# Kernel optimization log

Measured on AMD Instinct MI355X. Metric: run time of the kernel, lower is better.

Reference implementation:

```python
import jax, jax.numpy as jnp
import numpy as np
import math

B, S, H, D = 8, 4096, 768, 64  # batch, seq_len, hidden_dim, head_size


def setup_inputs() -> dict:
    key = jax.random.key(0)
    kx, kk, kq, kv, kbk, kbq, kbv = jax.random.split(key, 7)
    s = 1.0 / math.sqrt(H)
    return {
        "x": jax.random.normal(kx, (B, S, H), dtype=jnp.float32),
        "Wk": jax.random.normal(kk, (H, D), dtype=jnp.float32) * s,
        "bk": jax.random.normal(kbk, (D,), dtype=jnp.float32) * s,
        "Wq": jax.random.normal(kq, (H, D), dtype=jnp.float32) * s,
        "bq": jax.random.normal(kbq, (D,), dtype=jnp.float32) * s,
        "Wv": jax.random.normal(kv, (H, D), dtype=jnp.float32) * s,
        "bv": jax.random.normal(kbv, (D,), dtype=jnp.float32) * s,
    }


def reference(x, Wk, bk, Wq, bq, Wv, bv):
    # projections: [B, S, D]
    k = x @ Wk + bk
    q = x @ Wq + bq
    v = x @ Wv + bv
    # full O(S^2) attention scores, as in the original module
    weight = jnp.einsum("bqd,bkd->bqk", q, k)  # [B, S, S]
    causal = jnp.tril(jnp.ones((S, S), dtype=bool))
    # original masks first, then divides by sqrt(head_size); -inf/sqrt = -inf
    weight = jnp.where(causal, weight, -jnp.inf) / math.sqrt(D)
    weight = jax.nn.softmax(weight, axis=-1)
    # dropout p=0.0 (eval-mode reference): identity
    out = jnp.einsum("bqk,bkd->bqd", weight, v)  # [B, S, D]
    return out
```

## Files before the change

### kernel.cpp

```cpp
#include <hip/hip_runtime.h>
#include <hip/hip_bf16.h>
#include <math.h>

#define B_ 8
#define S_ 4096
#define H_ 768
#define D_ 64

typedef __bf16 bf16;
typedef bf16 bf16x8 __attribute__((ext_vector_type(8)));
typedef bf16 bf16x4 __attribute__((ext_vector_type(4)));
typedef float floatx4 __attribute__((ext_vector_type(4)));

__device__ __forceinline__ int sw_off(int r, int chunk) {
    return r * 128 + ((chunk ^ (r & 7)) << 4);
}
__device__ __forceinline__ int sw_elem(int r, int e) {
    return r * 64 + (((e >> 3) ^ (r & 7)) << 3) + (e & 7);
}

__device__ __forceinline__ void dma16(const bf16* gsrc, bf16* ldst) {
    __builtin_amdgcn_global_load_lds(
        (const __attribute__((address_space(1))) unsigned int*)(const void*)gsrc,
        (__attribute__((address_space(3))) unsigned int*)(void*)ldst,
        16, 0, 0);
}

__global__ __launch_bounds__(256) void wtrans_kernel(
    const float* __restrict__ Wq, const float* __restrict__ Wk,
    const float* __restrict__ Wv, bf16* __restrict__ wt)
{
    __shared__ bf16 t_lds[64][72];
    const float* W = (blockIdx.y == 0) ? Wq : (blockIdx.y == 1) ? Wk : Wv;
    bf16* o = wt + ((size_t)blockIdx.y * 12 + blockIdx.x) * 4096;
    const int k0 = blockIdx.x * 64;
    const int tid = threadIdx.x;
    #pragma unroll
    for (int rep = 0; rep < 16; ++rep) {
        int idx = rep * 256 + tid;
        int r = idx >> 6, n = idx & 63;
        t_lds[n][r] = (bf16)W[(size_t)(k0 + r) * D_ + n];
    }
    __syncthreads();
    #pragma unroll
    for (int rep = 0; rep < 16; ++rep) {
        int idx = rep * 256 + tid;
        int n = idx >> 6, kk = idx & 63;
        o[sw_elem(n, kk)] = t_lds[n][kk];
    }
}

__global__ __launch_bounds__(256, 2) void proj_kernel(
    const float* __restrict__ x, const bf16* __restrict__ wt,
    const float* __restrict__ bq, const float* __restrict__ bk,
    const float* __restrict__ bv,
    bf16* __restrict__ qout, bf16* __restrict__ kout, bf16* __restrict__ vtt)
{
    __shared__ bf16 wlds[2][3][4096];

    const int m0   = blockIdx.x * 64;
    const int tid  = threadIdx.x;
    const int lane = tid & 63;
    const int wave = tid >> 6;
    const int quad = lane >> 4;
    const int c    = lane & 15;
    const int mrow = m0 + wave * 16 + c;

    floatx4 acc[3][4] = {};
    const float* xrow = &x[(size_t)mrow * H_ + quad * 8];

    auto loadA = [&](int k0, bf16x8* dst) {
        #pragma unroll
        for (int s = 0; s < 2; ++s) {
            const float* xp = xrow + k0 + s * 32;
            float4 f0 = *(const float4*)xp;
            float4 f1 = *(const float4*)(xp + 4);
            bf16x8 a;
            a[0] = (bf16)f0.x; a[1] = (bf16)f0.y; a[2] = (bf16)f0.z; a[3] = (bf16)f0.w;
            a[4] = (bf16)f1.x; a[5] = (bf16)f1.y; a[6] = (bf16)f1.z; a[7] = (bf16)f1.w;
            dst[s] = a;
        }
    };
    auto stageW = [&](int kt, int buf) {
        #pragma unroll
        for (int w = 0; w < 3; ++w) {
            const bf16* src = wt + (size_t)(w * 12 + kt) * 4096 + wave * 1024 + lane * 8;
            bf16* dst = &wlds[buf][w][wave * 1024];
            dma16(src, dst);
            dma16(src + 512, dst + 512);
        }
    };

    bf16x8 afn[2]; loadA(0, afn);
    stageW(0, 0);

    for (int kt = 0; kt < 12; ++kt) {
        __syncthreads();
        const int cur = kt & 1;
        if (kt < 11) stageW(kt + 1, 1 - cur);
        bf16x8 af[2] = { afn[0], afn[1] };
        if (kt < 11) loadA((kt + 1) * 64, afn);
        #pragma unroll
        for (int s = 0; s < 2; ++s)
            #pragma unroll
            for (int w = 0; w < 3; ++w)
                #pragma unroll
                for (int tn = 0; tn < 4; ++tn) {
                    bf16x8 bfrag = *(const bf16x8*)
                        ((const char*)&wlds[cur][w][0] + sw_off(tn * 16 + c, s * 4 + quad));
                    acc[w][tn] = __builtin_amdgcn_mfma_f32_16x16x32_bf16(
                        af[s], bfrag, acc[w][tn], 0, 0, 0);
                }
    }

    const int rbase = m0 + wave * 16 + quad * 4;
    const int bb = m0 >> 12;
    const int jt = (m0 & 4095) >> 6;
    const size_t tbase = ((size_t)bb * 64 + jt) * 4096;
    #pragma unroll
    for (int tn = 0; tn < 4; ++tn) {
        const int n = tn * 16 + c;
        float bqv = bq[n];
        #pragma unroll
        for (int r = 0; r < 4; ++r)
            qout[(size_t)(rbase + r) * 128 + n] = (bf16)(acc[0][tn][r] + bqv);
        float bkv = bk[n];
        #pragma unroll
        for (int r = 0; r < 4; ++r) {
            const int sl = (rbase & 63) + r;
            kout[tbase + sw_elem(sl, n)] = (bf16)(acc[1][tn][r] + bkv);
        }
        float bvv = bv[n];
        bf16x4 pk;
        #pragma unroll
        for (int r = 0; r < 4; ++r) pk[r] = (bf16)(acc[2][tn][r] + bvv);
        const int sl0 = (rbase & 63);
        *(bf16x4*)&vtt[tbase + sw_elem(n, sl0)] = pk;
    }
}

__global__ __launch_bounds__(128, 2) void attn_kernel(
    const bf16* __restrict__ q, const bf16* __restrict__ k,
    const bf16* __restrict__ vt, float* __restrict__ out)
{
    __shared__ bf16 klds[2][4096];
    __shared__ bf16 vlds[2][4096];
    __shared__ bf16 plds[2][1024];

    const int tid  = threadIdx.x;
    const int lane = tid & 63;
    const int wave = tid >> 6;
    const int quad = lane >> 4;
    const int c    = lane & 15;
    const int i    = blockIdx.x;
    const int slot = i >> 8;
    const int cc   = i & 255;
    const int b    = cc & 7;
    const int x    = cc >> 3;
    const int qt   = (slot == 0) ? (127 - x) : (slot == 1) ? x
                   : (slot == 2) ? (95 - x)  : (32 + x);
    const int jmax = qt >> 1;
    const int qrow = qt * 32 + wave * 16;
    const float cl = 0.18033688011112042f;
    const float M2 = 16.0f;

    const bf16* ktile0 = k  + (size_t)b * 64 * 4096;
    const bf16* vtile0 = vt + (size_t)b * 64 * 4096;
    bf16* pl = &plds[wave][0];

    auto stage = [&](const bf16* gsrc, bf16* ldst) {
        const bf16* s = gsrc + wave * 2048 + lane * 8;
        bf16* d = ldst + wave * 2048;
        #pragma unroll
        for (int n = 0; n < 4; ++n) dma16(s + n * 512, d + n * 512);
    };

    bf16x8 qf[2];
    #pragma unroll
    for (int s = 0; s < 2; ++s)
        qf[s] = *(const bf16x8*)
            &q[(size_t)(b * S_ + qrow + c) * 128 + s * 32 + quad * 8];

    floatx4 acc_o[4] = {};
    float lpart[4] = {0.f, 0.f, 0.f, 0.f};

    stage(ktile0, klds[0]);
    stage(vtile0, vlds[0]);

    #pragma unroll 1
    for (int j = 0; j <= jmax; ++j) {
        __syncthreads();
        const int cur = j & 1;
        if (j < jmax) {
            stage(ktile0 + (size_t)(j + 1) * 4096, klds[1 - cur]);
            stage(vtile0 + (size_t)(j + 1) * 4096, vlds[1 - cur]);
        }

        floatx4 sa[4] = {};
        #pragma unroll
        for (int s = 0; s < 2; ++s)
            #pragma unroll
            for (int tn = 0; tn < 4; ++tn) {
                bf16x8 kf = *(const bf16x8*)
                    ((const char*)&klds[cur][0] + sw_off(tn * 16 + c, s * 4 + quad));
                sa[tn] = __builtin_amdgcn_mfma_f32_16x16x32_bf16(qf[s], kf, sa[tn], 0, 0, 0);
            }

        if (j == jmax) {
            #pragma unroll
            for (int tn = 0; tn < 4; ++tn) {
                const int col = j * 64 + tn * 16 + c;
                #pragma unroll
                for (int r = 0; r < 4; ++r)
                    if (col > qrow + quad * 4 + r) sa[tn][r] = -INFINITY;
            }
        }

        #pragma unroll
        for (int tn = 0; tn < 4; ++tn)
            #pragma unroll
            for (int r = 0; r < 4; ++r) {
                float p = __builtin_amdgcn_exp2f(fmaf(sa[tn][r], cl, -M2));
                sa[tn][r] = p;
                lpart[r] += p;
            }

        bf16x8 vf[2][4];
        #pragma unroll
        for (int s = 0; s < 2; ++s)
            #pragma unroll
            for (int tn = 0; tn < 4; ++tn)
                vf[s][tn] = *(const bf16x8*)
                    ((const char*)&vlds[cur][0] + sw_off(tn * 16 + c, s * 4 + quad));

        #pragma unroll
        for (int tn = 0; tn < 4; ++tn)
            #pragma unroll
            for (int r = 0; r < 4; ++r)
                pl[sw_elem(quad * 4 + r, tn * 16 + c)] = (bf16)sa[tn][r];

        bf16x8 pf[2];
        #pragma unroll
        for (int s = 0; s < 2; ++s)
            pf[s] = *(const bf16x8*)((const char*)pl + sw_off(c, s * 4 + quad));

        #pragma unroll
        for (int s = 0; s < 2; ++s)
            #pragma unroll
            for (int tn = 0; tn < 4; ++tn)
                acc_o[tn] = __builtin_amdgcn_mfma_f32_16x16x32_bf16(pf[s], vf[s][tn], acc_o[tn], 0, 0, 0);
    }

    #pragma unroll
    for (int r = 0; r < 4; ++r) {
        lpart[r] += __shfl_xor(lpart[r], 1);
        lpart[r] += __shfl_xor(lpart[r], 2);
        lpart[r] += __shfl_xor(lpart[r], 4);
        lpart[r] += __shfl_xor(lpart[r], 8);
    }

    float rl[4];
    #pragma unroll
    for (int r = 0; r < 4; ++r) rl[r] = 1.0f / lpart[r];
    #pragma unroll
    for (int tn = 0; tn < 4; ++tn)
        #pragma unroll
        for (int r = 0; r < 4; ++r)
            out[(size_t)(b * S_ + qrow + quad * 4 + r) * D_ + tn * 16 + c]
                = acc_o[tn][r] * rl[r];
}

extern "C" void kernel_launch(void* const* d_in, const int* in_sizes, int n_in,
                              void* d_out, int out_size, void* d_ws, size_t ws_size,
                              hipStream_t stream) {
    const float* x  = (const float*)d_in[0];
    const float* Wk = (const float*)d_in[1];
    const float* bk = (const float*)d_in[2];
    const float* Wq = (const float*)d_in[3];
    const float* bq = (const float*)d_in[4];
    const float* Wv = (const float*)d_in[5];
    const float* bv = (const float*)d_in[6];
    float* out = (float*)d_out;

    bf16* q_ws  = (bf16*)d_out;
    bf16* k_ws  = (bf16*)d_ws;
    bf16* vt_ws = k_ws + (size_t)B_ * S_ * D_;
    bf16* wt_ws = vt_ws + (size_t)B_ * S_ * D_;

    wtrans_kernel<<<dim3(H_ / 64, 3), 256, 0, stream>>>(Wq, Wk, Wv, wt_ws);
    proj_kernel<<<dim3(B_ * S_ / 64), 256, 0, stream>>>(
        x, wt_ws, bq, bk, bv, q_ws, k_ws, vt_ws);
    attn_kernel<<<dim3(1024), 128, 0, stream>>>(q_ws, k_ws, vt_ws, out);
}
```

Baseline: 232.2 us.

## Split KV for long causal query tiles, keep P in registers, add combine

The attention kernel now splits the KV range of the longer query tiles (the upper 64 tiles) into two halves across separate blocks. Each half writes an unnormalized partial output and a row sum to workspace, and a new combine kernel merges them. QK^T is computed transposed so the probabilities land directly in the B-operand layout of a 16x16x16 MFMA, which removes the LDS round trip for P. The projection kernel gains a deeper A prefetch and a higher occupancy hint. This trades an extra launch and partial-output traffic for better load balance and less LDS work per step.

```diff
diff --git a/kernel.cpp b/kernel.cpp
--- a/kernel.cpp
+++ b/kernel.cpp
@@ -11,6 +11,20 @@
 typedef bf16 bf16x8 __attribute__((ext_vector_type(8)));
 typedef bf16 bf16x4 __attribute__((ext_vector_type(4)));
 typedef float floatx4 __attribute__((ext_vector_type(4)));
+typedef short short4v __attribute__((ext_vector_type(4)));
+
+__device__ __forceinline__ floatx4 mfma16(bf16x4 a, bf16x4 b, floatx4 c) {
+#if __has_builtin(__builtin_amdgcn_mfma_f32_16x16x16_bf16)
+    return __builtin_amdgcn_mfma_f32_16x16x16_bf16(a, b, c, 0, 0, 0);
+#elif __has_builtin(__builtin_amdgcn_mfma_f32_16x16x16bf16_1k)
+    return __builtin_amdgcn_mfma_f32_16x16x16bf16_1k(
+        __builtin_bit_cast(short4v, a), __builtin_bit_cast(short4v, b), c, 0, 0, 0);
+#else
+    asm volatile("v_mfma_f32_16x16x16_bf16 %0, %1, %2, %0"
+                 : "+v"(c) : "v"(a), "v"(b));
+    return c;
+#endif
+}
 
 __device__ __forceinline__ int sw_off(int r, int chunk) {
     return r * 128 + ((chunk ^ (r & 7)) << 4);
@@ -50,7 +64,7 @@
     }
 }
 
-__global__ __launch_bounds__(256, 2) void proj_kernel(
+__global__ __launch_bounds__(256, 3) void proj_kernel(
     const float* __restrict__ x, const bf16* __restrict__ wt,
     const float* __restrict__ bq, const float* __restrict__ bk,
     const float* __restrict__ bv,
@@ -91,15 +105,17 @@
         }
     };
 
-    bf16x8 afn[2]; loadA(0, afn);
+    bf16x8 aA[2], aB[2];
+    loadA(0, aA); loadA(64, aB);
     stageW(0, 0);
 
     for (int kt = 0; kt < 12; ++kt) {
         __syncthreads();
         const int cur = kt & 1;
         if (kt < 11) stageW(kt + 1, 1 - cur);
-        bf16x8 af[2] = { afn[0], afn[1] };
-        if (kt < 11) loadA((kt + 1) * 64, afn);
+        bf16x8 af[2] = { aA[0], aA[1] };
+        aA[0] = aB[0]; aA[1] = aB[1];
+        if (kt < 10) loadA((kt + 2) * 64, aB);
         #pragma unroll
         for (int s = 0; s < 2; ++s)
             #pragma unroll
@@ -141,11 +157,11 @@
 
 __global__ __launch_bounds__(128, 2) void attn_kernel(
     const bf16* __restrict__ q, const bf16* __restrict__ k,
-    const bf16* __restrict__ vt, float* __restrict__ out)
+    const bf16* __restrict__ vt, float* __restrict__ out,
+    float* __restrict__ opart, float* __restrict__ lpws)
 {
     __shared__ bf16 klds[2][4096];
     __shared__ bf16 vlds[2][4096];
-    __shared__ bf16 plds[2][1024];
 
     const int tid  = threadIdx.x;
     const int lane = tid & 63;
@@ -153,20 +169,30 @@
     const int quad = lane >> 4;
     const int c    = lane & 15;
     const int i    = blockIdx.x;
-    const int slot = i >> 8;
-    const int cc   = i & 255;
-    const int b    = cc & 7;
-    const int x    = cc >> 3;
-    const int qt   = (slot == 0) ? (127 - x) : (slot == 1) ? x
-                   : (slot == 2) ? (95 - x)  : (32 + x);
-    const int jmax = qt >> 1;
+    const int b    = i & 7;
+
+    int qt, j0, jend, half = 0, split = 0;
+    if (i < 1024) {
+        const int u = i >> 3;
+        qt   = 127 - (u >> 1);
+        half = u & 1;
+        split = 1;
+        const int jmax = qt >> 1;
+        const int jmid = (jmax + 1) >> 1;
+        j0   = half ? jmid : 0;
+        jend = half ? jmax : (jmid - 1);
+    } else {
+        qt   = 63 - ((i - 1024) >> 3);
+        j0   = 0;
+        jend = qt >> 1;
+    }
+    const int jmax_diag = qt >> 1;
     const int qrow = qt * 32 + wave * 16;
     const float cl = 0.18033688011112042f;
     const float M2 = 16.0f;
 
     const bf16* ktile0 = k  + (size_t)b * 64 * 4096;
     const bf16* vtile0 = vt + (size_t)b * 64 * 4096;
-    bf16* pl = &plds[wave][0];
 
     auto stage = [&](const bf16* gsrc, bf16* ldst) {
         const bf16* s = gsrc + wave * 2048 + lane * 8;
@@ -182,16 +208,16 @@
             &q[(size_t)(b * S_ + qrow + c) * 128 + s * 32 + quad * 8];
 
     floatx4 acc_o[4] = {};
-    float lpart[4] = {0.f, 0.f, 0.f, 0.f};
-
-    stage(ktile0, klds[0]);
-    stage(vtile0, vlds[0]);
+    float lsum = 0.f;
+
+    stage(ktile0 + (size_t)j0 * 4096, klds[j0 & 1]);
+    stage(vtile0 + (size_t)j0 * 4096, vlds[j0 & 1]);
 
     #pragma unroll 1
-    for (int j = 0; j <= jmax; ++j) {
+    for (int j = j0; j <= jend; ++j) {
         __syncthreads();
         const int cur = j & 1;
-        if (j < jmax) {
+        if (j < jend) {
             stage(ktile0 + (size_t)(j + 1) * 4096, klds[1 - cur]);
             stage(vtile0 + (size_t)(j + 1) * 4096, vlds[1 - cur]);
         }
@@ -203,16 +229,24 @@
             for (int tn = 0; tn < 4; ++tn) {
                 bf16x8 kf = *(const bf16x8*)
                     ((const char*)&klds[cur][0] + sw_off(tn * 16 + c, s * 4 + quad));
-                sa[tn] = __builtin_amdgcn_mfma_f32_16x16x32_bf16(qf[s], kf, sa[tn], 0, 0, 0);
+                sa[tn] = __builtin_amdgcn_mfma_f32_16x16x32_bf16(kf, qf[s], sa[tn], 0, 0, 0);
             }
 
-        if (j == jmax) {
+        bf16x4 vfr[4][4];
+        #pragma unroll
+        for (int td = 0; td < 4; ++td)
+            #pragma unroll
+            for (int tn = 0; tn < 4; ++tn)
+                vfr[td][tn] = *(const bf16x4*)
+                    &vlds[cur][sw_elem(td * 16 + c, tn * 16 + quad * 4)];
+
+        if (j == jmax_diag) {
             #pragma unroll
             for (int tn = 0; tn < 4; ++tn) {
-                const int col = j * 64 + tn * 16 + c;
+                const int kvb = j * 64 + tn * 16 + quad * 4;
                 #pragma unroll
                 for (int r = 0; r < 4; ++r)
-                    if (col > qrow + quad * 4 + r) sa[tn][r] = -INFINITY;
+                    if (kvb + r > qrow + c) sa[tn][r] = -INFINITY;
             }
         }
 
@@ -222,52 +256,68 @@
             for (int r = 0; r < 4; ++r) {
                 float p = __builtin_amdgcn_exp2f(fmaf(sa[tn][r], cl, -M2));
                 sa[tn][r] = p;
-                lpart[r] += p;
+                lsum += p;
             }
 
-        bf16x8 vf[2][4];
-        #pragma unroll
-        for (int s = 0; s < 2; ++s)
-            #pragma unroll
-            for (int tn = 0; tn < 4; ++tn)
-                vf[s][tn] = *(const bf16x8*)
-                    ((const char*)&vlds[cur][0] + sw_off(tn * 16 + c, s * 4 + quad));
-
-        #pragma unroll
-        for (int tn = 0; tn < 4; ++tn)
-            #pragma unroll
-            for (int r = 0; r < 4; ++r)
-                pl[sw_elem(quad * 4 + r, tn * 16 + c)] = (bf16)sa[tn][r];
-
-        bf16x8 pf[2];
-        #pragma unroll
-        for (int s = 0; s < 2; ++s)
-            pf[s] = *(const bf16x8*)((const char*)pl + sw_off(c, s * 4 + quad));
-
-        #pragma unroll
-        for (int s = 0; s < 2; ++s)
-            #pragma unroll
-            for (int tn = 0; tn < 4; ++tn)
-                acc_o[tn] = __builtin_amdgcn_mfma_f32_16x16x32_bf16(pf[s], vf[s][tn], acc_o[tn], 0, 0, 0);
-    }
-
-    #pragma unroll
-    for (int r = 0; r < 4; ++r) {
-        lpart[r] += __shfl_xor(lpart[r], 1);
-        lpart[r] += __shfl_xor(lpart[r], 2);
-        lpart[r] += __shfl_xor(lpart[r], 4);
-        lpart[r] += __shfl_xor(lpart[r], 8);
-    }
-
-    float rl[4];
-    #pragma unroll
-    for (int r = 0; r < 4; ++r) rl[r] = 1.0f / lpart[r];
-    #pragma unroll
-    for (int tn = 0; tn < 4; ++tn)
-        #pragma unroll
-        for (int r = 0; r < 4; ++r)
-            out[(size_t)(b * S_ + qrow + quad * 4 + r) * D_ + tn * 16 + c]
-                = acc_o[tn][r] * rl[r];
+        #pragma unroll
+        for (int tn = 0; tn < 4; ++tn) {
+            bf16x4 pb;
+            #pragma unroll
+            for (int r = 0; r < 4; ++r) pb[r] = (bf16)sa[tn][r];
+            #pragma unroll
+            for (int td = 0; td < 4; ++td)
+                acc_o[td] = mfma16(vfr[td][tn], pb, acc_o[td]);
+        }
+    }
+
+    lsum += __shfl_xor(lsum, 16);
+    lsum += __shfl_xor(lsum, 32);
+
+    if (!split) {
+        const float rl = 1.0f / lsum;
+        #pragma unroll
+        for (int td = 0; td < 4; ++td) {
+            floatx4 v = acc_o[td] * rl;
+            *(float4*)&out[(size_t)(b * S_ + qrow + c) * 64 + td * 16 + quad * 4]
+                = *(float4*)&v;
+        }
+    } else {
+        const int tile = qt - 64;
+        const int row  = wave * 16 + c;
+        float* op = opart + ((((size_t)half * 8 + b) * 64 + tile) * 32) * 64;
+        #pragma unroll
+        for (int td = 0; td < 4; ++td)
+            *(float4*)&op[row * 64 + td * 16 + quad * 4] = *(float4*)&acc_o[td];
+        if (quad == 0)
+            lpws[(((size_t)half * 8 + b) * 64 + tile) * 32 + row] = lsum;
+    }
+}
+
+__global__ __launch_bounds__(256) void combine_kernel(
+    const float* __restrict__ opart, const float* __restrict__ lpws,
+    float* __restrict__ out)
+{
+    const int b    = blockIdx.x & 7;
+    const int tile = blockIdx.x >> 3;
+    const int tid  = threadIdx.x;
+    const int row  = tid >> 3;
+    const int c8   = (tid & 7) * 8;
+
+    const size_t ti = ((size_t)b * 64 + tile) * 32 + row;
+    const float rl = 1.0f / (lpws[ti] + lpws[(size_t)8 * 64 * 32 + ti]);
+
+    const size_t oa = (((size_t)b * 64 + tile) * 32 + row) * 64 + c8;
+    const size_t ob = (size_t)8 * 64 * 32 * 64 + oa;
+    const size_t oo = (size_t)(b * S_ + (64 + tile) * 32 + row) * 64 + c8;
+    #pragma unroll
+    for (int h = 0; h < 2; ++h) {
+        float4 a = *(const float4*)&opart[oa + h * 4];
+        float4 bb = *(const float4*)&opart[ob + h * 4];
+        float4 o;
+        o.x = (a.x + bb.x) * rl; o.y = (a.y + bb.y) * rl;
+        o.z = (a.z + bb.z) * rl; o.w = (a.w + bb.w) * rl;
+        *(float4*)&out[oo + h * 4] = o;
+    }
 }
 
 extern "C" void kernel_launch(void* const* d_in, const int* in_sizes, int n_in,
@@ -286,9 +336,12 @@
     bf16* k_ws  = (bf16*)d_ws;
     bf16* vt_ws = k_ws + (size_t)B_ * S_ * D_;
     bf16* wt_ws = vt_ws + (size_t)B_ * S_ * D_;
+    float* opart = (float*)(wt_ws + 3 * 12 * 4096);
+    float* lpws  = opart + (size_t)2 * 8 * 64 * 32 * 64;
 
     wtrans_kernel<<<dim3(H_ / 64, 3), 256, 0, stream>>>(Wq, Wk, Wv, wt_ws);
     proj_kernel<<<dim3(B_ * S_ / 64), 256, 0, stream>>>(
         x, wt_ws, bq, bk, bv, q_ws, k_ws, vt_ws);
-    attn_kernel<<<dim3(1024), 128, 0, stream>>>(q_ws, k_ws, vt_ws, out);
-}
+    attn_kernel<<<dim3(1536), 128, 0, stream>>>(q_ws, k_ws, vt_ws, out, opart, lpws);
+    combine_kernel<<<dim3(512), 256, 0, stream>>>(opart, lpws, out);
+}
```

Measured after the change: 215.1 us. 1.08x faster.
